# Kernel optimization log

Hardware: AMD Instinct MI355X
Metric: run time of the kernel (lower is better)

## Reference

```python
import jax, jax.numpy as jnp
import numpy as np

EMB_DIM = 1024
HEAD_NUM = 16
HEAD_DIM = EMB_DIM // HEAD_NUM
B, S = 2, 2048


def setup_inputs() -> dict:
    key = jax.random.key(0)
    k_x, k_wqkv, k_bqkv, k_wo, k_bo = jax.random.split(key, 5)
    x = jax.random.normal(k_x, (B, S, EMB_DIM), dtype=jnp.float32)
    # nn.Linear default init scale ~ 1/sqrt(fan_in); exact distribution irrelevant for a reference
    lim = 1.0 / np.sqrt(EMB_DIM)
    W_qkv = jax.random.uniform(k_wqkv, (EMB_DIM, 3 * EMB_DIM), jnp.float32, -lim, lim)
    b_qkv = jax.random.uniform(k_bqkv, (3 * EMB_DIM,), jnp.float32, -lim, lim)
    W_o = jax.random.uniform(k_wo, (EMB_DIM, EMB_DIM), jnp.float32, -lim, lim)
    b_o = jax.random.uniform(k_bo, (EMB_DIM,), jnp.float32, -lim, lim)
    mask = jnp.tril(jnp.ones((S, S), dtype=bool))  # causal mask as in casual_mask(seq_len)
    return {"x": x, "W_qkv": W_qkv, "b_qkv": b_qkv, "W_o": W_o, "b_o": b_o, "mask": mask}


def reference(x, W_qkv, b_qkv, W_o, b_o, mask):
    b, s, e = x.shape
    qkv = x @ W_qkv + b_qkv                      # [b, s, 3e]
    q, k, v = qkv[..., :e], qkv[..., e:2 * e], qkv[..., 2 * e:]
    # [b, s, h, d] -> [b, h, s, d]
    q = q.reshape(b, s, HEAD_NUM, HEAD_DIM).transpose(0, 2, 1, 3)
    k = k.reshape(b, s, HEAD_NUM, HEAD_DIM).transpose(0, 2, 1, 3)
    v = v.reshape(b, s, HEAD_NUM, HEAD_DIM).transpose(0, 2, 1, 3)
    scores = jnp.einsum("bhqd,bhkd->bhqk", q, k) / jnp.sqrt(jnp.float32(HEAD_DIM))
    scores = jnp.where(mask, scores, -jnp.inf)   # masked_fill(~mask, -inf)
    probs = jax.nn.softmax(scores, axis=-1)      # dropout is identity in eval mode
    out = jnp.einsum("bhqk,bhkd->bhqd", probs, v)
    out = out.transpose(0, 2, 1, 3).reshape(b, s, e)
    return out @ W_o + b_o
```

## Files before the change

### kernel.cpp

```cpp
#include <hip/hip_runtime.h>


typedef __attribute__((ext_vector_type(8))) short short8;
typedef __attribute__((ext_vector_type(4))) float floatx4;

#define NB 2
#define SEQ 2048
#define EMB 1024
#define NH 16
#define HD 64
#define M_ROWS (NB * SEQ)
#define N_QKV (3 * EMB)
#define SLOT_F 4160

#define GLL(g, l) __builtin_amdgcn_global_load_lds( \
    (const __attribute__((address_space(1))) void*)(g), \
    (__attribute__((address_space(3))) void*)(l), 16, 0, 0)

static __device__ __forceinline__ unsigned short f2bf(float f) {
    union { float f; unsigned int u; } v; v.f = f;
    unsigned int r = v.u + 0x7FFFu + ((v.u >> 16) & 1u);
    return (unsigned short)(r >> 16);
}

__global__ void x_to_bf16(const float* __restrict__ in, unsigned short* __restrict__ out, int n4) {
    int i = blockIdx.x * blockDim.x + threadIdx.x;
    if (i >= n4) return;
    float4 v = ((const float4*)in)[i];
    unsigned long long p = (unsigned long long)f2bf(v.x)
        | ((unsigned long long)f2bf(v.y) << 16)
        | ((unsigned long long)f2bf(v.z) << 32)
        | ((unsigned long long)f2bf(v.w) << 48);
    ((unsigned long long*)out)[i] = p;
}

__global__ void transpose_weights(const float* __restrict__ Wqkv, const float* __restrict__ Wo,
                                  unsigned short* __restrict__ wqkvT, unsigned short* __restrict__ woT) {
    __shared__ unsigned short tile[32][33];
    int z = blockIdx.z;
    int C = z ? EMB : N_QKV;
    if ((int)blockIdx.x * 32 >= C) return;
    const float* in = z ? Wo : Wqkv;
    unsigned short* out = z ? woT : wqkvT;
    const int R = EMB;
    int tx = threadIdx.x, ty = threadIdx.y;
    int c0 = blockIdx.x * 32, r0 = blockIdx.y * 32;
    #pragma unroll
    for (int j = 0; j < 4; ++j)
        tile[ty + j * 8][tx] = f2bf(in[(size_t)(r0 + ty + j * 8) * C + c0 + tx]);
    __syncthreads();
    #pragma unroll
    for (int j = 0; j < 4; ++j)
        out[(size_t)(c0 + ty + j * 8) * R + r0 + tx] = tile[tx][ty + j * 8];
}

#define CTS 130

__global__ __launch_bounds__(256) void qkv_gemm(
    const unsigned short* __restrict__ A,
    const unsigned short* __restrict__ Bt,
    const float* __restrict__ bias,
    unsigned short* __restrict__ qb, unsigned short* __restrict__ kb,
    unsigned short* __restrict__ vb)
{
    const int K = EMB;
    __shared__ __align__(16) unsigned short smem[128 * CTS];

    int t = threadIdx.x;
    int m0 = blockIdx.y * 128;
    int n0 = blockIdx.x * 128;
    int w = t >> 6, lane = t & 63, quad = lane >> 4, lcol = lane & 15;
    int wr = w >> 1, wc = w & 1;

    floatx4 zero = {0.f, 0.f, 0.f, 0.f};
    floatx4 acc[4][4];
    #pragma unroll
    for (int i = 0; i < 4; ++i)
        #pragma unroll
        for (int j = 0; j < 4; ++j) acc[i][j] = zero;

    const unsigned short* a0 = A  + (size_t)(m0 + (t >> 2)) * K + ((t & 3) << 3);
    const unsigned short* b0 = Bt + (size_t)(n0 + (t >> 2)) * K + ((t & 3) << 3);
    unsigned short* la = &smem[t << 3];

    GLL(a0, la);
    GLL(a0 + 64 * K, la + 2048);
    GLL(b0, la + 4096);
    GLL(b0 + 64 * K, la + 6144);

    for (int k0 = 0; k0 < K; k0 += 32) {
        int cur = (k0 >> 5) & 1, nxt = cur ^ 1;
        __syncthreads();
        if (k0 + 32 < K) {
            GLL(a0 + k0 + 32, la + nxt * 8192);
            GLL(a0 + 64 * K + k0 + 32, la + nxt * 8192 + 2048);
            GLL(b0 + k0 + 32, la + nxt * 8192 + 4096);
            GLL(b0 + 64 * K + k0 + 32, la + nxt * 8192 + 6144);
        }
        const unsigned short* As = &smem[cur * 8192];
        const unsigned short* Bs = As + 4096;
        short8 af[4], bfm[4];
        #pragma unroll
        for (int i = 0; i < 4; ++i)
            af[i] = *(const short8*)(&As[(wr * 64 + i * 16 + lcol) * 32 + quad * 8]);
        #pragma unroll
        for (int j = 0; j < 4; ++j)
            bfm[j] = *(const short8*)(&Bs[(wc * 64 + j * 16 + lcol) * 32 + quad * 8]);
        #pragma unroll
        for (int i = 0; i < 4; ++i)
            #pragma unroll
            for (int j = 0; j < 4; ++j)
                acc[i][j] = __builtin_amdgcn_mfma_f32_16x16x32_bf16(af[i], bfm[j], acc[i][j], 0, 0, 0);
    }

    bool isV = (n0 >= 2 * EMB);
    __syncthreads();
    #pragma unroll
    for (int i = 0; i < 4; ++i) {
        int row0 = wr * 64 + i * 16 + quad * 4;
        #pragma unroll
        for (int j = 0; j < 4; ++j) {
            int col = wc * 64 + j * 16 + lcol;
            float bv = bias[n0 + col];
            #pragma unroll
            for (int r = 0; r < 4; ++r) {
                unsigned short hv = f2bf(acc[i][j][r] + bv);
                if (isV) smem[col * CTS + row0 + r] = hv;
                else     smem[(row0 + r) * CTS + col] = hv;
            }
        }
    }
    __syncthreads();

    int b = m0 >> 11, s0 = m0 & 2047;
    int hbase = (n0 & 1023) >> 6;
    if (!isV) {
        unsigned short* dst = (n0 >= EMB) ? kb : qb;
        #pragma unroll
        for (int it = 0; it < 8; ++it) {
            int job = it * 32 + (t >> 3);
            int tok = job & 127, hh = job >> 7;
            int chunk = t & 7;
            short8 vv = *(const short8*)(&smem[tok * CTS + hh * 64 + chunk * 8]);
            size_t g = ((size_t)((b * NH + hbase + hh) * SEQ + s0 + tok)) * HD + chunk * 8;
            *(short8*)(&dst[g]) = vv;
        }
    } else {
        #pragma unroll
        for (int it = 0; it < 8; ++it) {
            int job = it * 32 + (t >> 3);
            int f = job & 127, half = job >> 7;
            int chunk = (t & 7) + half * 8;
            short8 vv = *(const short8*)(&smem[f * CTS + chunk * 8]);
            int h = hbase + (f >> 6), d = f & 63;
            size_t g = ((size_t)((b * NH + h) * HD + d)) * SEQ + s0 + chunk * 8;
            *(short8*)(&vb[g]) = vv;
        }
    }
}

#define PST 68

__global__ __launch_bounds__(256) void attn_partial(
    const unsigned short* __restrict__ Q,
    const unsigned short* __restrict__ Kk,
    const unsigned short* __restrict__ Vt,
    unsigned short* __restrict__ Out,
    float* __restrict__ Part)
{
    __shared__ __align__(16) unsigned short Ks[2][64 * 64];
    __shared__ __align__(16) unsigned short Vs[2][64 * 64];
    __shared__ __align__(16) unsigned short Ps[4][16 * PST];

    int u = blockIdx.x;
    int bh = blockIdx.y;
    int qt, c;
    if (u < 16) { qt = u; c = 0; }
    else { int v = u - 16; qt = 16 + (v >> 1); c = v & 1; }
    int ktBeg = c << 4;
    int ktEnd = (c == 0 && qt >= 16) ? 16 : (qt + 1);

    int q0 = qt * 64;
    int t = threadIdx.x;
    int w = t >> 6, lane = t & 63, quad = lane >> 4, lcol = lane & 15;
    const size_t hoff = (size_t)bh * SEQ * HD;
    const float SC = 0.18033688011112043f;

    const unsigned short* qp = Q + hoff + (size_t)(q0 + 16 * w + lcol) * HD + quad * 8;
    short8 aq0 = *(const short8*)qp, aq1 = *(const short8*)(qp + 32);

    int srow = t >> 3;
    int ss   = (t & 7) ^ (srow & 7);
    const unsigned short* kgl = Kk + hoff + (size_t)srow * HD + ss * 8;
    const unsigned short* vgl = Vt + hoff + (size_t)srow * SEQ + ss * 8;
    unsigned short* kld = &Ks[0][t * 8];
    unsigned short* vld = &Vs[0][t * 8];

    floatx4 zero = {0.f, 0.f, 0.f, 0.f};
    floatx4 O[4];
    float l[4] = {0.f, 0.f, 0.f, 0.f};
    #pragma unroll
    for (int d = 0; d < 4; ++d) O[d] = zero;

    {
        int k0 = ktBeg * 64;
        GLL(kgl + (size_t)k0 * HD, kld);
        GLL(kgl + (size_t)(k0 + 32) * HD, kld + 2048);
        GLL(vgl + k0, vld);
        GLL(vgl + (size_t)32 * SEQ + k0, vld + 2048);
    }

    int sx0 = (quad ^ (lcol & 7)) << 3;
    int sx1 = sx0 ^ 32;

    for (int kt = ktBeg; kt < ktEnd; ++kt) {
        int cur = kt & 1, nxt = cur ^ 1;
        __syncthreads();
        if (kt + 1 < ktEnd) {
            int k0 = (kt + 1) * 64;
            GLL(kgl + (size_t)k0 * HD, kld + nxt * 4096);
            GLL(kgl + (size_t)(k0 + 32) * HD, kld + nxt * 4096 + 2048);
            GLL(vgl + k0, vld + nxt * 4096);
            GLL(vgl + (size_t)32 * SEQ + k0, vld + nxt * 4096 + 2048);
        }

        const unsigned short* ksr = &Ks[cur][0];
        const unsigned short* vsr = &Vs[cur][0];
        short8 bk0[4], bk1[4], bv0[4], bv1[4];
        #pragma unroll
        for (int tc = 0; tc < 4; ++tc) {
            int rb = (tc * 16 + lcol) << 6;
            bk0[tc] = *(const short8*)(ksr + rb + sx0);
            bk1[tc] = *(const short8*)(ksr + rb + sx1);
            bv0[tc] = *(const short8*)(vsr + rb + sx0);
            bv1[tc] = *(const short8*)(vsr + rb + sx1);
        }

        floatx4 sacc[4];
        #pragma unroll
        for (int tc = 0; tc < 4; ++tc) {
            sacc[tc] = __builtin_amdgcn_mfma_f32_16x16x32_bf16(aq0, bk0[tc], zero, 0, 0, 0);
            sacc[tc] = __builtin_amdgcn_mfma_f32_16x16x32_bf16(aq1, bk1[tc], sacc[tc], 0, 0, 0);
        }
        unsigned short* PsW = &Ps[w][0];
        if (kt == qt) {
            int rbase = 16 * w + quad * 4;
            #pragma unroll
            for (int tc = 0; tc < 4; ++tc) {
                int keyc = tc * 16 + lcol;
                #pragma unroll
                for (int r = 0; r < 4; ++r) {
                    float p = __builtin_amdgcn_exp2f(sacc[tc][r] * SC);
                    if (keyc > rbase + r) p = 0.f;
                    l[r] += p;
                    PsW[(quad * 4 + r) * PST + keyc] = f2bf(p);
                }
            }
        } else {
            #pragma unroll
            for (int tc = 0; tc < 4; ++tc) {
                int keyc = tc * 16 + lcol;
                #pragma unroll
                for (int r = 0; r < 4; ++r) {
                    float p = __builtin_amdgcn_exp2f(sacc[tc][r] * SC);
                    l[r] += p;
                    PsW[(quad * 4 + r) * PST + keyc] = f2bf(p);
                }
            }
        }
        short8 ap0 = *(const short8*)(&PsW[lcol * PST + quad * 8]);
        short8 ap1 = *(const short8*)(&PsW[lcol * PST + 32 + quad * 8]);
        #pragma unroll
        for (int td = 0; td < 4; ++td) {
            O[td] = __builtin_amdgcn_mfma_f32_16x16x32_bf16(ap0, bv0[td], O[td], 0, 0, 0);
            O[td] = __builtin_amdgcn_mfma_f32_16x16x32_bf16(ap1, bv1[td], O[td], 0, 0, 0);
        }
    }

    #pragma unroll
    for (int r = 0; r < 4; ++r) {
        #pragma unroll
        for (int off = 1; off < 16; off <<= 1)
            l[r] += __shfl_xor(l[r], off, 64);
    }

    if (qt < 16) {
        int b = bh >> 4, h = bh & 15;
        size_t obase = ((size_t)b * SEQ) * EMB + (size_t)h * HD;
        #pragma unroll
        for (int td = 0; td < 4; ++td) {
            #pragma unroll
            for (int r = 0; r < 4; ++r) {
                int row = q0 + 16 * w + quad * 4 + r;
                Out[obase + (size_t)row * EMB + td * 16 + lcol] = f2bf(O[td][r] / l[r]);
            }
        }
    } else {
        float* slot = Part + ((size_t)(bh * 16 + (qt - 16)) * 2 + c) * SLOT_F;
        #pragma unroll
        for (int td = 0; td < 4; ++td) {
            #pragma unroll
            for (int r = 0; r < 4; ++r)
                slot[(16 * w + quad * 4 + r) * 64 + td * 16 + lcol] = O[td][r];
        }
        if (lcol == 0) {
            #pragma unroll
            for (int r = 0; r < 4; ++r)
                slot[4096 + 16 * w + quad * 4 + r] = l[r];
        }
    }
}

__global__ __launch_bounds__(256) void attn_combine(
    const float* __restrict__ Part, unsigned short* __restrict__ Out)
{
    int qh = blockIdx.x;
    int bh = blockIdx.y;
    int qt = 16 + qh;
    const float* s0 = Part + ((size_t)(bh * 16 + qh) * 2) * SLOT_F;
    const float* s1 = s0 + SLOT_F;
    int b = bh >> 4, h = bh & 15;
    size_t obase = ((size_t)b * SEQ + qt * 64) * EMB + (size_t)h * HD;
    int t = threadIdx.x;
    #pragma unroll
    for (int it = 0; it < 16; ++it) {
        int idx = it * 256 + t;
        int row = idx >> 6, col = idx & 63;
        float lv = s0[4096 + row] + s1[4096 + row];
        float v = (s0[idx] + s1[idx]) / lv;
        Out[obase + (size_t)row * EMB + col] = f2bf(v);
    }
}

__global__ __launch_bounds__(256) void oproj_gemm(
    const unsigned short* __restrict__ A,
    const unsigned short* __restrict__ Bt,
    const float* __restrict__ bias,
    float* __restrict__ Cout)
{
    const int K = EMB;
    __shared__ __align__(16) unsigned short smem[2 * 8192];
    int t = threadIdx.x;
    int m0 = blockIdx.y * 128;
    int n0 = blockIdx.x * 128;
    int w = t >> 6, lane = t & 63, quad = lane >> 4, lcol = lane & 15;
    int wr = w >> 1, wc = w & 1;

    floatx4 zero = {0.f, 0.f, 0.f, 0.f};
    floatx4 acc[4][4];
    #pragma unroll
    for (int i = 0; i < 4; ++i)
        #pragma unroll
        for (int j = 0; j < 4; ++j) acc[i][j] = zero;

    const unsigned short* a0 = A  + (size_t)(m0 + (t >> 2)) * K + ((t & 3) << 3);
    const unsigned short* b0 = Bt + (size_t)(n0 + (t >> 2)) * K + ((t & 3) << 3);
    unsigned short* la = &smem[t << 3];

    GLL(a0, la);
    GLL(a0 + 64 * K, la + 2048);
    GLL(b0, la + 4096);
    GLL(b0 + 64 * K, la + 6144);

    for (int k0 = 0; k0 < K; k0 += 32) {
        int cur = (k0 >> 5) & 1, nxt = cur ^ 1;
        __syncthreads();
        if (k0 + 32 < K) {
            GLL(a0 + k0 + 32, la + nxt * 8192);
            GLL(a0 + 64 * K + k0 + 32, la + nxt * 8192 + 2048);
            GLL(b0 + k0 + 32, la + nxt * 8192 + 4096);
            GLL(b0 + 64 * K + k0 + 32, la + nxt * 8192 + 6144);
        }
        const unsigned short* As = &smem[cur * 8192];
        const unsigned short* Bs = As + 4096;
        short8 af[4], bfm[4];
        #pragma unroll
        for (int i = 0; i < 4; ++i)
            af[i] = *(const short8*)(&As[(wr * 64 + i * 16 + lcol) * 32 + quad * 8]);
        #pragma unroll
        for (int j = 0; j < 4; ++j)
            bfm[j] = *(const short8*)(&Bs[(wc * 64 + j * 16 + lcol) * 32 + quad * 8]);
        #pragma unroll
        for (int i = 0; i < 4; ++i)
            #pragma unroll
            for (int j = 0; j < 4; ++j)
                acc[i][j] = __builtin_amdgcn_mfma_f32_16x16x32_bf16(af[i], bfm[j], acc[i][j], 0, 0, 0);
    }

    #pragma unroll
    for (int i = 0; i < 4; ++i) {
        int m = m0 + wr * 64 + i * 16 + quad * 4;
        #pragma unroll
        for (int j = 0; j < 4; ++j) {
            int n = n0 + wc * 64 + j * 16 + lcol;
            float bv = bias[n];
            #pragma unroll
            for (int r = 0; r < 4; ++r)
                Cout[(size_t)(m + r) * EMB + n] = acc[i][j][r] + bv;
        }
    }
}

extern "C" void kernel_launch(void* const* d_in, const int* in_sizes, int n_in,
                              void* d_out, int out_size, void* d_ws, size_t ws_size,
                              hipStream_t stream) {
    (void)in_sizes; (void)n_in; (void)out_size; (void)ws_size;
    char* ws = (char*)d_ws;
    const size_t OFF_X     = 0;
    const size_t OFF_WQKVT = OFF_X     + (size_t)M_ROWS * EMB * 2;
    const size_t OFF_WOT   = OFF_WQKVT + (size_t)N_QKV * EMB * 2;
    const size_t OFF_Q     = OFF_WOT   + (size_t)EMB * EMB * 2;
    const size_t OFF_K     = OFF_Q     + (size_t)M_ROWS * EMB * 2;
    const size_t OFF_V     = OFF_K     + (size_t)M_ROWS * EMB * 2;
    const size_t OFF_ATTN  = OFF_V     + (size_t)M_ROWS * EMB * 2;
    const size_t OFF_PART  = OFF_ATTN  + (size_t)M_ROWS * EMB * 2;

    const float* x    = (const float*)d_in[0];
    const float* Wqkv = (const float*)d_in[1];
    const float* bqkv = (const float*)d_in[2];
    const float* Wo   = (const float*)d_in[3];
    const float* bo   = (const float*)d_in[4];

    unsigned short* x_bf  = (unsigned short*)(ws + OFF_X);
    unsigned short* wqkvT = (unsigned short*)(ws + OFF_WQKVT);
    unsigned short* woT   = (unsigned short*)(ws + OFF_WOT);
    unsigned short* qb    = (unsigned short*)(ws + OFF_Q);
    unsigned short* kb    = (unsigned short*)(ws + OFF_K);
    unsigned short* vb    = (unsigned short*)(ws + OFF_V);
    unsigned short* attn  = (unsigned short*)(ws + OFF_ATTN);
    float*          part  = (float*)(ws + OFF_PART);

    x_to_bf16<<<(M_ROWS * EMB / 4 + 255) / 256, 256, 0, stream>>>(x, x_bf, M_ROWS * EMB / 4);
    transpose_weights<<<dim3(N_QKV / 32, EMB / 32, 2), dim3(32, 8), 0, stream>>>(Wqkv, Wo, wqkvT, woT);

    qkv_gemm<<<dim3(N_QKV / 128, M_ROWS / 128), 256, 0, stream>>>(x_bf, wqkvT, bqkv, qb, kb, vb);
    attn_partial<<<dim3(48, NB * NH), 256, 0, stream>>>(qb, kb, vb, attn, part);
    attn_combine<<<dim3(16, NB * NH), 256, 0, stream>>>(part, attn);
    oproj_gemm<<<dim3(EMB / 128, M_ROWS / 128), 256, 0, stream>>>(attn, woT, bo, (float*)d_out);
}
```

Measured before the change: 217.9 us.

## Merge prep kernels, compute softmax row sums via MFMA, store partials as bf16

Folds the x-to-bf16 conversion into the weight-transpose kernel as a third grid slice, which removes one kernel launch. In attention, the per-row softmax denominator is now computed with extra MFMAs against a vector of ones instead of scalar adds plus cross-lane shuffles. Split-K partial outputs are stored as bf16 rather than fp32 to halve the traffic of the combine step, with the division replaced by a reciprocal multiply. In exchange, the partials lose precision, and the row sums now use the bf16-rounded probabilities.

```diff
diff --git a/kernel.cpp b/kernel.cpp
--- a/kernel.cpp
+++ b/kernel.cpp
@@ -11,7 +11,7 @@
 #define HD 64
 #define M_ROWS (NB * SEQ)
 #define N_QKV (3 * EMB)
-#define SLOT_F 4160
+#define SLOT_B 8448
 
 #define GLL(g, l) __builtin_amdgcn_global_load_lds( \
     (const __attribute__((address_space(1))) void*)(g), \
@@ -22,28 +22,36 @@
     unsigned int r = v.u + 0x7FFFu + ((v.u >> 16) & 1u);
     return (unsigned short)(r >> 16);
 }
-
-__global__ void x_to_bf16(const float* __restrict__ in, unsigned short* __restrict__ out, int n4) {
-    int i = blockIdx.x * blockDim.x + threadIdx.x;
-    if (i >= n4) return;
-    float4 v = ((const float4*)in)[i];
-    unsigned long long p = (unsigned long long)f2bf(v.x)
-        | ((unsigned long long)f2bf(v.y) << 16)
-        | ((unsigned long long)f2bf(v.z) << 32)
-        | ((unsigned long long)f2bf(v.w) << 48);
-    ((unsigned long long*)out)[i] = p;
-}
-
-__global__ void transpose_weights(const float* __restrict__ Wqkv, const float* __restrict__ Wo,
-                                  unsigned short* __restrict__ wqkvT, unsigned short* __restrict__ woT) {
+static __device__ __forceinline__ float bf2f(unsigned short h) {
+    union { unsigned int u; float f; } v; v.u = ((unsigned int)h) << 16;
+    return v.f;
+}
+
+__global__ void prep(const float* __restrict__ x,
+                     const float* __restrict__ Wqkv, const float* __restrict__ Wo,
+                     unsigned short* __restrict__ x_bf,
+                     unsigned short* __restrict__ wqkvT, unsigned short* __restrict__ woT) {
     __shared__ unsigned short tile[32][33];
     int z = blockIdx.z;
+    int tx = threadIdx.x, ty = threadIdx.y;
+    if (z == 2) {
+        int id = ((int)blockIdx.y * 96 + (int)blockIdx.x) * 256 + ty * 32 + tx;
+        const int n4 = M_ROWS * EMB / 4;
+        for (int i = id; i < n4; i += 96 * 32 * 256) {
+            float4 v = ((const float4*)x)[i];
+            unsigned long long p = (unsigned long long)f2bf(v.x)
+                | ((unsigned long long)f2bf(v.y) << 16)
+                | ((unsigned long long)f2bf(v.z) << 32)
+                | ((unsigned long long)f2bf(v.w) << 48);
+            ((unsigned long long*)x_bf)[i] = p;
+        }
+        return;
+    }
     int C = z ? EMB : N_QKV;
     if ((int)blockIdx.x * 32 >= C) return;
     const float* in = z ? Wo : Wqkv;
     unsigned short* out = z ? woT : wqkvT;
     const int R = EMB;
-    int tx = threadIdx.x, ty = threadIdx.y;
     int c0 = blockIdx.x * 32, r0 = blockIdx.y * 32;
     #pragma unroll
     for (int j = 0; j < 4; ++j)
@@ -166,7 +174,7 @@
     const unsigned short* __restrict__ Kk,
     const unsigned short* __restrict__ Vt,
     unsigned short* __restrict__ Out,
-    float* __restrict__ Part)
+    unsigned char* __restrict__ Part)
 {
     __shared__ __align__(16) unsigned short Ks[2][64 * 64];
     __shared__ __align__(16) unsigned short Vs[2][64 * 64];
@@ -198,9 +206,13 @@
 
     floatx4 zero = {0.f, 0.f, 0.f, 0.f};
     floatx4 O[4];
-    float l[4] = {0.f, 0.f, 0.f, 0.f};
+    floatx4 lacc = zero;
     #pragma unroll
     for (int d = 0; d < 4; ++d) O[d] = zero;
+
+    short8 ones;
+    #pragma unroll
+    for (int j = 0; j < 8; ++j) ones[j] = (short)0x3F80;
 
     {
         int k0 = ktBeg * 64;
@@ -252,7 +264,6 @@
                 for (int r = 0; r < 4; ++r) {
                     float p = __builtin_amdgcn_exp2f(sacc[tc][r] * SC);
                     if (keyc > rbase + r) p = 0.f;
-                    l[r] += p;
                     PsW[(quad * 4 + r) * PST + keyc] = f2bf(p);
                 }
             }
@@ -263,7 +274,6 @@
                 #pragma unroll
                 for (int r = 0; r < 4; ++r) {
                     float p = __builtin_amdgcn_exp2f(sacc[tc][r] * SC);
-                    l[r] += p;
                     PsW[(quad * 4 + r) * PST + keyc] = f2bf(p);
                 }
             }
@@ -275,50 +285,54 @@
             O[td] = __builtin_amdgcn_mfma_f32_16x16x32_bf16(ap0, bv0[td], O[td], 0, 0, 0);
             O[td] = __builtin_amdgcn_mfma_f32_16x16x32_bf16(ap1, bv1[td], O[td], 0, 0, 0);
         }
-    }
-
-    #pragma unroll
-    for (int r = 0; r < 4; ++r) {
-        #pragma unroll
-        for (int off = 1; off < 16; off <<= 1)
-            l[r] += __shfl_xor(l[r], off, 64);
+        lacc = __builtin_amdgcn_mfma_f32_16x16x32_bf16(ap0, ones, lacc, 0, 0, 0);
+        lacc = __builtin_amdgcn_mfma_f32_16x16x32_bf16(ap1, ones, lacc, 0, 0, 0);
     }
 
     if (qt < 16) {
         int b = bh >> 4, h = bh & 15;
         size_t obase = ((size_t)b * SEQ) * EMB + (size_t)h * HD;
+        float inv[4];
+        #pragma unroll
+        for (int r = 0; r < 4; ++r) inv[r] = 1.0f / lacc[r];
         #pragma unroll
         for (int td = 0; td < 4; ++td) {
             #pragma unroll
             for (int r = 0; r < 4; ++r) {
                 int row = q0 + 16 * w + quad * 4 + r;
-                Out[obase + (size_t)row * EMB + td * 16 + lcol] = f2bf(O[td][r] / l[r]);
+                Out[obase + (size_t)row * EMB + td * 16 + lcol] = f2bf(O[td][r] * inv[r]);
             }
         }
     } else {
-        float* slot = Part + ((size_t)(bh * 16 + (qt - 16)) * 2 + c) * SLOT_F;
+        unsigned char* sp = Part + ((size_t)(bh * 16 + (qt - 16)) * 2 + c) * SLOT_B;
+        unsigned short* sO = (unsigned short*)sp;
+        float* sL = (float*)(sp + 8192);
         #pragma unroll
         for (int td = 0; td < 4; ++td) {
             #pragma unroll
             for (int r = 0; r < 4; ++r)
-                slot[(16 * w + quad * 4 + r) * 64 + td * 16 + lcol] = O[td][r];
+                sO[(16 * w + quad * 4 + r) * 64 + td * 16 + lcol] = f2bf(O[td][r]);
         }
         if (lcol == 0) {
             #pragma unroll
             for (int r = 0; r < 4; ++r)
-                slot[4096 + 16 * w + quad * 4 + r] = l[r];
+                sL[16 * w + quad * 4 + r] = lacc[r];
         }
     }
 }
 
 __global__ __launch_bounds__(256) void attn_combine(
-    const float* __restrict__ Part, unsigned short* __restrict__ Out)
+    const unsigned char* __restrict__ Part, unsigned short* __restrict__ Out)
 {
     int qh = blockIdx.x;
     int bh = blockIdx.y;
     int qt = 16 + qh;
-    const float* s0 = Part + ((size_t)(bh * 16 + qh) * 2) * SLOT_F;
-    const float* s1 = s0 + SLOT_F;
+    const unsigned char* s0 = Part + ((size_t)(bh * 16 + qh) * 2) * SLOT_B;
+    const unsigned char* s1 = s0 + SLOT_B;
+    const unsigned short* O0 = (const unsigned short*)s0;
+    const unsigned short* O1 = (const unsigned short*)s1;
+    const float* L0 = (const float*)(s0 + 8192);
+    const float* L1 = (const float*)(s1 + 8192);
     int b = bh >> 4, h = bh & 15;
     size_t obase = ((size_t)b * SEQ + qt * 64) * EMB + (size_t)h * HD;
     int t = threadIdx.x;
@@ -326,8 +340,8 @@
     for (int it = 0; it < 16; ++it) {
         int idx = it * 256 + t;
         int row = idx >> 6, col = idx & 63;
-        float lv = s0[4096 + row] + s1[4096 + row];
-        float v = (s0[idx] + s1[idx]) / lv;
+        float lv = L0[row] + L1[row];
+        float v = (bf2f(O0[idx]) + bf2f(O1[idx])) / lv;
         Out[obase + (size_t)row * EMB + col] = f2bf(v);
     }
 }
@@ -428,10 +442,9 @@
     unsigned short* kb    = (unsigned short*)(ws + OFF_K);
     unsigned short* vb    = (unsigned short*)(ws + OFF_V);
     unsigned short* attn  = (unsigned short*)(ws + OFF_ATTN);
-    float*          part  = (float*)(ws + OFF_PART);
-
-    x_to_bf16<<<(M_ROWS * EMB / 4 + 255) / 256, 256, 0, stream>>>(x, x_bf, M_ROWS * EMB / 4);
-    transpose_weights<<<dim3(N_QKV / 32, EMB / 32, 2), dim3(32, 8), 0, stream>>>(Wqkv, Wo, wqkvT, woT);
+    unsigned char*  part  = (unsigned char*)(ws + OFF_PART);
+
+    prep<<<dim3(96, 32, 3), dim3(32, 8), 0, stream>>>(x, Wqkv, Wo, x_bf, wqkvT, woT);
 
     qkv_gemm<<<dim3(N_QKV / 128, M_ROWS / 128), 256, 0, stream>>>(x_bf, wqkvT, bqkv, qb, kb, vb);
     attn_partial<<<dim3(48, NB * NH), 256, 0, stream>>>(qb, kb, vb, attn, part);
```

After: 212.5 us. 1.03x faster.
